# Performance work log

Measured on AMD Instinct MI355X. Metric: run time of the kernel, lower is better.

The kernel has to match this reference:

```python
import jax, jax.numpy as jnp
import numpy as np

B, T, E = 2, 2048, 1024
H = 16
HS = E // H  # 64
EPS = 1e-5


def _ln(x, g, b):
    mu = jnp.mean(x, axis=-1, keepdims=True)
    var = jnp.mean((x - mu) ** 2, axis=-1, keepdims=True)
    return (x - mu) * jax.lax.rsqrt(var + EPS) * g + b


def setup_inputs() -> dict:
    key = jax.random.key(0)
    ks = jax.random.split(key, 12)
    s_e = 1.0 / np.sqrt(E)
    s_h = 1.0 / np.sqrt(H * HS)
    s_f = 1.0 / np.sqrt(4 * E)
    return {
        "x": jax.random.normal(ks[0], (B, T, E), jnp.float32),
        # per-head Q/K/V weights stacked: [H, E, HS] (Linear bias=False)
        "Wq": jax.random.uniform(ks[1], (H, E, HS), jnp.float32, -s_e, s_e),
        "Wk": jax.random.uniform(ks[2], (H, E, HS), jnp.float32, -s_e, s_e),
        "Wv": jax.random.uniform(ks[3], (H, E, HS), jnp.float32, -s_e, s_e),
        # output projection: [H*HS, E]
        "Wp": jax.random.uniform(ks[4], (H * HS, E), jnp.float32, -s_h, s_h),
        "bp": jax.random.uniform(ks[5], (E,), jnp.float32, -s_h, s_h),
        # FFN
        "W1": jax.random.uniform(ks[6], (E, 4 * E), jnp.float32, -s_e, s_e),
        "b1": jax.random.uniform(ks[7], (4 * E,), jnp.float32, -s_e, s_e),
        "W2": jax.random.uniform(ks[8], (4 * E, E), jnp.float32, -s_f, s_f),
        "b2": jax.random.uniform(ks[9], (E,), jnp.float32, -s_f, s_f),
        # LayerNorms
        "g1": jnp.ones((E,), jnp.float32),
        "beta1": jnp.zeros((E,), jnp.float32),
        "g2": jnp.ones((E,), jnp.float32),
        "beta2": jnp.zeros((E,), jnp.float32),
    }


def reference(x, Wq, Wk, Wv, Wp, bp, W1, b1, W2, b2, g1, beta1, g2, beta2):
    # --- pre-LN + multi-head causal self-attention ---
    h = _ln(x, g1, beta1)                                   # [B,T,E]
    Q = jnp.einsum('bte,hed->bhtd', h, Wq)                  # [B,H,T,HS]
    K = jnp.einsum('bte,hed->bhtd', h, Wk)
    V = jnp.einsum('bte,hed->bhtd', h, Wv)
    scores = jnp.einsum('bhtd,bhsd->bhts', Q, K) * (HS ** -0.5)  # [B,H,T,T]
    mask = jnp.tril(jnp.ones((T, T), bool))
    scores = jnp.where(mask, scores, -jnp.inf)
    W = jax.nn.softmax(scores, axis=-1)                     # dropout p=0.0
    out = jnp.einsum('bhts,bhsd->bhtd', W, V)               # [B,H,T,HS]
    out = out.transpose(0, 2, 1, 3).reshape(B, T, H * HS)   # concat heads
    x = x + out @ Wp + bp                                   # residual 1
    # --- pre-LN + FFN ---
    h2 = _ln(x, g2, beta2)
    ff = jax.nn.relu(h2 @ W1 + b1) @ W2 + b2
    return x + ff
```

## Files before the change

kernel.cpp:

```cpp
#include <hip/hip_runtime.h>
#include <math.h>
#include <stdint.h>

typedef unsigned short u16;
typedef __attribute__((ext_vector_type(8))) short bf16x8;
typedef __attribute__((ext_vector_type(4))) float f32x4;

__device__ __forceinline__ u16 f2bf(float f) {
  unsigned int u = __float_as_uint(f);
  u += 0x7FFFu + ((u >> 16) & 1u);
  return (u16)(u >> 16);
}

__global__ __launch_bounds__(256) void transpose_bf16(
    const float* __restrict__ src, u16* __restrict__ dst,
    int R, int C, long sbs, long dbs, int drs, float scale) {
  __shared__ float tile[32][33];
  int c0 = blockIdx.x * 32, r0 = blockIdx.y * 32;
  long sb = (long)blockIdx.z * sbs, db = (long)blockIdx.z * dbs;
  int tx = threadIdx.x & 31, ty = threadIdx.x >> 5;
  #pragma unroll
  for (int k = 0; k < 4; ++k)
    tile[ty + k * 8][tx] = src[sb + (long)(r0 + ty + k * 8) * C + c0 + tx];
  __syncthreads();
  #pragma unroll
  for (int k = 0; k < 4; ++k)
    dst[db + (long)(c0 + ty + k * 8) * drs + r0 + tx] =
        f2bf(tile[tx][ty + k * 8] * scale);
}

__global__ __launch_bounds__(256) void vtrans(
    const u16* __restrict__ QKV, u16* __restrict__ VT) {
  __shared__ u16 Tl[64][72];
  int bt = blockIdx.x, h = blockIdx.y;
  int t = threadIdx.x;
  int r = t >> 3, c0 = (t & 7) << 3;
  const u16* src = QKV + (size_t)(bt * 64 + r) * 3072 + 2048 + h * 64 + c0;
  #pragma unroll
  for (int half = 0; half < 2; ++half) {
    bf16x8 v = *(const bf16x8*)(src + (size_t)(half * 32) * 3072);
    #pragma unroll
    for (int e = 0; e < 8; ++e) Tl[r + half * 32][c0 + e] = (u16)v[e];
  }
  __syncthreads();
  #pragma unroll
  for (int half = 0; half < 2; ++half) {
    int d = (t >> 3) + half * 32, s0 = (t & 7) << 3;
    bf16x8 o;
    #pragma unroll
    for (int e = 0; e < 8; ++e) o[e] = (short)Tl[s0 + e][d];
    *(bf16x8*)(VT + (size_t)(h * 64 + d) * 4096 + bt * 64 + s0) = o;
  }
}

__global__ __launch_bounds__(256) void ln_bf16(
    const float* __restrict__ x, const float* __restrict__ g,
    const float* __restrict__ b, u16* __restrict__ out) {
  int row = blockIdx.x;
  const float* xr = x + (size_t)row * 1024;
  int t = threadIdx.x;
  float4 v = *(const float4*)(xr + t * 4);
  float s = v.x + v.y + v.z + v.w;
  float q = v.x * v.x + v.y * v.y + v.z * v.z + v.w * v.w;
  #pragma unroll
  for (int off = 32; off >= 1; off >>= 1) {
    s += __shfl_xor(s, off);
    q += __shfl_xor(q, off);
  }
  __shared__ float ss[4], qq[4];
  int wid = t >> 6;
  if ((t & 63) == 0) { ss[wid] = s; qq[wid] = q; }
  __syncthreads();
  float st = ss[0] + ss[1] + ss[2] + ss[3];
  float qt = qq[0] + qq[1] + qq[2] + qq[3];
  float mean = st * (1.0f / 1024.0f);
  float var = qt * (1.0f / 1024.0f) - mean * mean;
  float rstd = rsqrtf(var + 1e-5f);
  float4 gv = *(const float4*)(g + t * 4);
  float4 bv = *(const float4*)(b + t * 4);
  u16 o0 = f2bf((v.x - mean) * rstd * gv.x + bv.x);
  u16 o1 = f2bf((v.y - mean) * rstd * gv.y + bv.y);
  u16 o2 = f2bf((v.z - mean) * rstd * gv.z + bv.z);
  u16 o3 = f2bf((v.w - mean) * rstd * gv.w + bv.w);
  uint2 st2;
  st2.x = (unsigned)o0 | ((unsigned)o1 << 16);
  st2.y = (unsigned)o2 | ((unsigned)o3 << 16);
  *(uint2*)(out + (size_t)row * 1024 + t * 4) = st2;
}

template <int BM, int BN>
__global__ __launch_bounds__(256) void gemm_bf16(
    const u16* __restrict__ A, const u16* __restrict__ Bt,
    const float* __restrict__ bias, const float* __restrict__ res,
    float* __restrict__ Cf, u16* __restrict__ Cb,
    int M, int N, int K, int relu) {
  constexpr int MI = BM / 32, NI = BN / 32;
  constexpr int ACH = BM / 32, BCH = BN / 32;
  __shared__ u16 As[2][BM * 64];
  __shared__ u16 Bs[2][BN * 64];
  int tid = threadIdx.x, wave = tid >> 6, lane = tid & 63;
  int wm = wave >> 1, wn = wave & 1;
  int lr = lane & 15, lq = lane >> 4;
  int lrow = lane >> 3, kblk = (lane & 7) ^ (lrow & 7);
  int bn = blockIdx.x * BN, bm = blockIdx.y * BM;
  f32x4 acc[MI][NI];
  #pragma unroll
  for (int i = 0; i < MI; ++i)
    #pragma unroll
    for (int j = 0; j < NI; ++j) acc[i][j] = f32x4{0.f, 0.f, 0.f, 0.f};

  const u16* ag[ACH];
  #pragma unroll
  for (int j = 0; j < ACH; ++j) {
    int c = wave * ACH + j;
    ag[j] = A + (size_t)(bm + c * 8 + lrow) * K + kblk * 8;
  }
  const u16* bg[BCH];
  #pragma unroll
  for (int j = 0; j < BCH; ++j) {
    int c = wave * BCH + j;
    bg[j] = Bt + (size_t)(bn + c * 8 + lrow) * K + kblk * 8;
  }

  bf16x8 ra[ACH], rb[BCH];
  #pragma unroll
  for (int j = 0; j < ACH; ++j) ra[j] = *(const bf16x8*)(ag[j]);
  #pragma unroll
  for (int j = 0; j < BCH; ++j) rb[j] = *(const bf16x8*)(bg[j]);

  int nIter = K >> 6;
  for (int it = 0; it < nIter; ++it) {
    int buf = it & 1;
    #pragma unroll
    for (int j = 0; j < ACH; ++j)
      *(bf16x8*)(&As[buf][(wave * ACH + j) * 512 + lane * 8]) = ra[j];
    #pragma unroll
    for (int j = 0; j < BCH; ++j)
      *(bf16x8*)(&Bs[buf][(wave * BCH + j) * 512 + lane * 8]) = rb[j];
    __syncthreads();
    if (it + 1 < nIter) {
      int k0 = (it + 1) << 6;
      #pragma unroll
      for (int j = 0; j < ACH; ++j) ra[j] = *(const bf16x8*)(ag[j] + k0);
      #pragma unroll
      for (int j = 0; j < BCH; ++j) rb[j] = *(const bf16x8*)(bg[j] + k0);
    }
    #pragma unroll
    for (int kk = 0; kk < 2; ++kk) {
      bf16x8 af[MI], bfr[NI];
      #pragma unroll
      for (int mi = 0; mi < MI; ++mi) {
        int row = wm * (BM / 2) + mi * 16 + lr;
        af[mi] = *(const bf16x8*)(&As[buf][row * 64 + (((kk << 2) + lq) ^ (lr & 7)) * 8]);
      }
      #pragma unroll
      for (int ni = 0; ni < NI; ++ni) {
        int row = wn * (BN / 2) + ni * 16 + lr;
        bfr[ni] = *(const bf16x8*)(&Bs[buf][row * 64 + (((kk << 2) + lq) ^ (lr & 7)) * 8]);
      }
      #pragma unroll
      for (int mi = 0; mi < MI; ++mi)
        #pragma unroll
        for (int ni = 0; ni < NI; ++ni)
          acc[mi][ni] = __builtin_amdgcn_mfma_f32_16x16x32_bf16(af[mi], bfr[ni], acc[mi][ni], 0, 0, 0);
    }
  }

  #pragma unroll
  for (int mi = 0; mi < MI; ++mi) {
    #pragma unroll
    for (int r = 0; r < 4; ++r) {
      int row = bm + wm * (BM / 2) + mi * 16 + lq * 4 + r;
      #pragma unroll
      for (int ni = 0; ni < NI; ++ni) {
        int col = bn + wn * (BN / 2) + ni * 16 + lr;
        float v = acc[mi][ni][r];
        if (bias) v += bias[col];
        if (res) v += res[(size_t)row * N + col];
        if (relu) v = fmaxf(v, 0.f);
        if (Cb) Cb[(size_t)row * N + col] = f2bf(v);
        else Cf[(size_t)row * N + col] = v;
      }
    }
  }
}

__global__ __launch_bounds__(256) void attn_mfma(
    const u16* __restrict__ QKV, const u16* __restrict__ VT,
    u16* __restrict__ O) {
  __shared__ u16 Klds[2][64 * 64];
  __shared__ u16 Vl[2][64 * 64];
  __shared__ u16 Pl[4][16][72];
  int qt = 31 - blockIdx.x;
  int b = blockIdx.y >> 4, hh = blockIdx.y & 15;
  int tid = threadIdx.x, wave = tid >> 6, lane = tid & 63;
  int lr = lane & 15, lq = lane >> 4;
  int lrow = lane >> 3, kb = (lane & 7) ^ (lrow & 7);

  int qrow = qt * 64 + wave * 16 + lr;
  const u16* qp = QKV + (size_t)(b * 2048 + qrow) * 3072 + hh * 64 + lq * 8;
  bf16x8 qf0 = *(const bf16x8*)qp;
  bf16x8 qf1 = *(const bf16x8*)(qp + 32);

  f32x4 of[4];
  float lsum[4];
  #pragma unroll
  for (int i = 0; i < 4; ++i) { of[i] = f32x4{0.f, 0.f, 0.f, 0.f}; lsum[i] = 0.f; }

  const u16* kg[2];
  const u16* vg[2];
  #pragma unroll
  for (int j = 0; j < 2; ++j) {
    int c = wave * 2 + j;
    kg[j] = QKV + (size_t)(b * 2048 + c * 8 + lrow) * 3072 + 1024 + hh * 64 + kb * 8;
    vg[j] = VT + (size_t)(hh * 64 + c * 8 + lrow) * 4096 + b * 2048 + kb * 8;
  }

  bf16x8 rk[2], rv[2];
  #pragma unroll
  for (int j = 0; j < 2; ++j) {
    rk[j] = *(const bf16x8*)(kg[j]);
    rv[j] = *(const bf16x8*)(vg[j]);
  }

  for (int kt = 0; kt <= qt; ++kt) {
    int buf = kt & 1;
    #pragma unroll
    for (int j = 0; j < 2; ++j) {
      *(bf16x8*)(&Klds[buf][(wave * 2 + j) * 512 + lane * 8]) = rk[j];
      *(bf16x8*)(&Vl[buf][(wave * 2 + j) * 512 + lane * 8]) = rv[j];
    }
    __syncthreads();
    if (kt < qt) {
      #pragma unroll
      for (int j = 0; j < 2; ++j) {
        rk[j] = *(const bf16x8*)(kg[j] + (size_t)(kt + 1) * 64 * 3072);
        rv[j] = *(const bf16x8*)(vg[j] + (kt + 1) * 64);
      }
    }

    f32x4 sf[4];
    #pragma unroll
    for (int i = 0; i < 4; ++i) sf[i] = f32x4{0.f, 0.f, 0.f, 0.f};
    #pragma unroll
    for (int ni = 0; ni < 4; ++ni) {
      int row = ni * 16 + lr;
      bf16x8 k0 = *(const bf16x8*)(&Klds[buf][row * 64 + ((lq) ^ (lr & 7)) * 8]);
      bf16x8 k1 = *(const bf16x8*)(&Klds[buf][row * 64 + ((4 + lq) ^ (lr & 7)) * 8]);
      sf[ni] = __builtin_amdgcn_mfma_f32_16x16x32_bf16(qf0, k0, sf[ni], 0, 0, 0);
      sf[ni] = __builtin_amdgcn_mfma_f32_16x16x32_bf16(qf1, k1, sf[ni], 0, 0, 0);
    }
    if (kt == qt) {
      #pragma unroll
      for (int ni = 0; ni < 4; ++ni) {
        int col = ni * 16 + lr;
        #pragma unroll
        for (int r = 0; r < 4; ++r) {
          int row = wave * 16 + lq * 4 + r;
          if (col > row) sf[ni][r] = -1e30f;
        }
      }
    }
    #pragma unroll
    for (int ni = 0; ni < 4; ++ni)
      #pragma unroll
      for (int r = 0; r < 4; ++r) {
        float p = exp2f(sf[ni][r]);
        sf[ni][r] = p;
        lsum[r] += p;
        Pl[wave][lq * 4 + r][ni * 16 + lr] = f2bf(p);
      }
    bf16x8 pa0 = *(const bf16x8*)(&Pl[wave][lr][lq * 8]);
    bf16x8 pa1 = *(const bf16x8*)(&Pl[wave][lr][32 + lq * 8]);
    #pragma unroll
    for (int ni = 0; ni < 4; ++ni) {
      int row = ni * 16 + lr;
      bf16x8 v0 = *(const bf16x8*)(&Vl[buf][row * 64 + ((lq) ^ (lr & 7)) * 8]);
      bf16x8 v1 = *(const bf16x8*)(&Vl[buf][row * 64 + ((4 + lq) ^ (lr & 7)) * 8]);
      of[ni] = __builtin_amdgcn_mfma_f32_16x16x32_bf16(pa0, v0, of[ni], 0, 0, 0);
      of[ni] = __builtin_amdgcn_mfma_f32_16x16x32_bf16(pa1, v1, of[ni], 0, 0, 0);
    }
  }
  #pragma unroll
  for (int r = 0; r < 4; ++r) {
    float l = lsum[r];
    l += __shfl_xor(l, 1);
    l += __shfl_xor(l, 2);
    l += __shfl_xor(l, 4);
    l += __shfl_xor(l, 8);
    float inv = 1.0f / l;
    int row = qt * 64 + wave * 16 + lq * 4 + r;
    u16* op = O + (size_t)(b * 2048 + row) * 1024 + hh * 64;
    #pragma unroll
    for (int ni = 0; ni < 4; ++ni)
      op[ni * 16 + lr] = f2bf(of[ni][r] * inv);
  }
}

extern "C" void kernel_launch(void* const* d_in, const int* in_sizes, int n_in,
                              void* d_out, int out_size, void* d_ws, size_t ws_size,
                              hipStream_t stream) {
  const float* x   = (const float*)d_in[0];
  const float* Wq  = (const float*)d_in[1];
  const float* Wk  = (const float*)d_in[2];
  const float* Wv  = (const float*)d_in[3];
  const float* Wp  = (const float*)d_in[4];
  const float* bp  = (const float*)d_in[5];
  const float* W1  = (const float*)d_in[6];
  const float* b1  = (const float*)d_in[7];
  const float* W2  = (const float*)d_in[8];
  const float* b2  = (const float*)d_in[9];
  const float* g1  = (const float*)d_in[10];
  const float* be1 = (const float*)d_in[11];
  const float* g2  = (const float*)d_in[12];
  const float* be2 = (const float*)d_in[13];
  float* out = (float*)d_out;

  u16* ws16   = (u16*)d_ws;
  u16* Wqkv_t = ws16;
  u16* Wp_t   = Wqkv_t + 3145728;
  u16* W1_t   = Wp_t + 1048576;
  u16* W2_t   = W1_t + 4194304;
  u16* h      = W2_t + 4194304;
  u16* QKV    = h + 4194304;
  u16* Obuf   = QKV + 12582912;
  u16* f      = QKV;
  float* x1   = (float*)(Obuf + 4194304);
  u16* VT     = (u16*)(x1 + 4194304);

  const float qsc = 0.18033688f;
  transpose_bf16<<<dim3(2, 32, 16), 256, 0, stream>>>(Wq, Wqkv_t, 1024, 64, 65536, 65536, 1024, qsc);
  transpose_bf16<<<dim3(2, 32, 16), 256, 0, stream>>>(Wk, Wqkv_t + 1048576, 1024, 64, 65536, 65536, 1024, 1.f);
  transpose_bf16<<<dim3(2, 32, 16), 256, 0, stream>>>(Wv, Wqkv_t + 2097152, 1024, 64, 65536, 65536, 1024, 1.f);
  transpose_bf16<<<dim3(32, 32, 1), 256, 0, stream>>>(Wp, Wp_t, 1024, 1024, 0, 0, 1024, 1.f);
  transpose_bf16<<<dim3(128, 32, 1), 256, 0, stream>>>(W1, W1_t, 1024, 4096, 0, 0, 1024, 1.f);
  transpose_bf16<<<dim3(32, 128, 1), 256, 0, stream>>>(W2, W2_t, 4096, 1024, 0, 0, 4096, 1.f);

  ln_bf16<<<4096, 256, 0, stream>>>(x, g1, be1, h);
  gemm_bf16<128, 128><<<dim3(24, 32), 256, 0, stream>>>(h, Wqkv_t, nullptr, nullptr,
                                                        nullptr, QKV, 4096, 3072, 1024, 0);
  vtrans<<<dim3(64, 16), 256, 0, stream>>>(QKV, VT);
  attn_mfma<<<dim3(32, 32), 256, 0, stream>>>(QKV, VT, Obuf);
  gemm_bf16<128, 64><<<dim3(16, 32), 256, 0, stream>>>(Obuf, Wp_t, bp, x,
                                                       x1, nullptr, 4096, 1024, 1024, 0);
  ln_bf16<<<4096, 256, 0, stream>>>(x1, g2, be2, h);
  gemm_bf16<128, 128><<<dim3(32, 32), 256, 0, stream>>>(h, W1_t, b1, nullptr,
                                                        nullptr, f, 4096, 4096, 1024, 1);
  gemm_bf16<128, 64><<<dim3(16, 32), 256, 0, stream>>>(f, W2_t, b2, x1,
                                                       out, nullptr, 4096, 1024, 4096, 0);
}
```

Baseline: 415.1 us.

## Pair causal attention query tiles, double-buffer GEMM registers, vectorize epilogues

Attention blocks now handle two query tiles (i and 31-i), so every block does the same amount of causal work and each loaded K/V tile serves both. The grid is halved. The GEMM main loop is unrolled by two with two register prefetch sets, loading two k-steps ahead. MFMA operands are swapped so each lane holds four consecutive columns, which allows vectorized bias/residual loads and packed bf16/float4 stores. Rounding changes from round-to-nearest-even to a cheaper add-and-perm packing, and register pressure rises in both kernels.

```diff
diff --git a/kernel.cpp b/kernel.cpp
--- a/kernel.cpp
+++ b/kernel.cpp
@@ -10,6 +10,12 @@
   unsigned int u = __float_as_uint(f);
   u += 0x7FFFu + ((u >> 16) & 1u);
   return (u16)(u >> 16);
+}
+
+__device__ __forceinline__ unsigned pkbf(float a, float b) {
+  unsigned ua = __float_as_uint(a) + 0x8000u;
+  unsigned ub = __float_as_uint(b) + 0x8000u;
+  return __builtin_amdgcn_perm(ub, ua, 0x07060302u);
 }
 
 __global__ __launch_bounds__(256) void transpose_bf16(
@@ -78,13 +84,9 @@
   float rstd = rsqrtf(var + 1e-5f);
   float4 gv = *(const float4*)(g + t * 4);
   float4 bv = *(const float4*)(b + t * 4);
-  u16 o0 = f2bf((v.x - mean) * rstd * gv.x + bv.x);
-  u16 o1 = f2bf((v.y - mean) * rstd * gv.y + bv.y);
-  u16 o2 = f2bf((v.z - mean) * rstd * gv.z + bv.z);
-  u16 o3 = f2bf((v.w - mean) * rstd * gv.w + bv.w);
   uint2 st2;
-  st2.x = (unsigned)o0 | ((unsigned)o1 << 16);
-  st2.y = (unsigned)o2 | ((unsigned)o3 << 16);
+  st2.x = pkbf((v.x - mean) * rstd * gv.x + bv.x, (v.y - mean) * rstd * gv.y + bv.y);
+  st2.y = pkbf((v.z - mean) * rstd * gv.z + bv.z, (v.w - mean) * rstd * gv.w + bv.w);
   *(uint2*)(out + (size_t)row * 1024 + t * 4) = st2;
 }
 
@@ -122,64 +124,75 @@
     bg[j] = Bt + (size_t)(bn + c * 8 + lrow) * K + kblk * 8;
   }
 
-  bf16x8 ra[ACH], rb[BCH];
-  #pragma unroll
-  for (int j = 0; j < ACH; ++j) ra[j] = *(const bf16x8*)(ag[j]);
-  #pragma unroll
-  for (int j = 0; j < BCH; ++j) rb[j] = *(const bf16x8*)(bg[j]);
+  bf16x8 ra0[ACH], ra1[ACH], rb0[BCH], rb1[BCH];
+  #pragma unroll
+  for (int j = 0; j < ACH; ++j) { ra0[j] = *(const bf16x8*)(ag[j]); ra1[j] = *(const bf16x8*)(ag[j] + 64); }
+  #pragma unroll
+  for (int j = 0; j < BCH; ++j) { rb0[j] = *(const bf16x8*)(bg[j]); rb1[j] = *(const bf16x8*)(bg[j] + 64); }
 
   int nIter = K >> 6;
-  for (int it = 0; it < nIter; ++it) {
-    int buf = it & 1;
-    #pragma unroll
-    for (int j = 0; j < ACH; ++j)
-      *(bf16x8*)(&As[buf][(wave * ACH + j) * 512 + lane * 8]) = ra[j];
-    #pragma unroll
-    for (int j = 0; j < BCH; ++j)
-      *(bf16x8*)(&Bs[buf][(wave * BCH + j) * 512 + lane * 8]) = rb[j];
-    __syncthreads();
-    if (it + 1 < nIter) {
-      int k0 = (it + 1) << 6;
-      #pragma unroll
-      for (int j = 0; j < ACH; ++j) ra[j] = *(const bf16x8*)(ag[j] + k0);
-      #pragma unroll
-      for (int j = 0; j < BCH; ++j) rb[j] = *(const bf16x8*)(bg[j] + k0);
-    }
-    #pragma unroll
-    for (int kk = 0; kk < 2; ++kk) {
-      bf16x8 af[MI], bfr[NI];
-      #pragma unroll
-      for (int mi = 0; mi < MI; ++mi) {
-        int row = wm * (BM / 2) + mi * 16 + lr;
-        af[mi] = *(const bf16x8*)(&As[buf][row * 64 + (((kk << 2) + lq) ^ (lr & 7)) * 8]);
-      }
-      #pragma unroll
-      for (int ni = 0; ni < NI; ++ni) {
-        int row = wn * (BN / 2) + ni * 16 + lr;
-        bfr[ni] = *(const bf16x8*)(&Bs[buf][row * 64 + (((kk << 2) + lq) ^ (lr & 7)) * 8]);
-      }
-      #pragma unroll
-      for (int mi = 0; mi < MI; ++mi)
+
+#define GEMM_STEP(BUF, RA, RB, IT)                                                         \
+  {                                                                                        \
+    _Pragma("unroll") for (int j = 0; j < ACH; ++j)                                        \
+        *(bf16x8*)(&As[BUF][(wave * ACH + j) * 512 + lane * 8]) = RA[j];                   \
+    _Pragma("unroll") for (int j = 0; j < BCH; ++j)                                        \
+        *(bf16x8*)(&Bs[BUF][(wave * BCH + j) * 512 + lane * 8]) = RB[j];                   \
+    __syncthreads();                                                                       \
+    if ((IT) + 2 < nIter) {                                                                \
+      int k0 = ((IT) + 2) << 6;                                                            \
+      _Pragma("unroll") for (int j = 0; j < ACH; ++j) RA[j] = *(const bf16x8*)(ag[j] + k0); \
+      _Pragma("unroll") for (int j = 0; j < BCH; ++j) RB[j] = *(const bf16x8*)(bg[j] + k0); \
+    }                                                                                      \
+    _Pragma("unroll") for (int kk = 0; kk < 2; ++kk) {                                     \
+      bf16x8 af[MI], bfr[NI];                                                              \
+      _Pragma("unroll") for (int mi = 0; mi < MI; ++mi)                                    \
+          af[mi] = *(const bf16x8*)(&As[BUF][(wm * (BM / 2) + mi * 16 + lr) * 64 +         \
+                                             (((kk << 2) + lq) ^ (lr & 7)) * 8]);          \
+      _Pragma("unroll") for (int ni = 0; ni < NI; ++ni)                                    \
+          bfr[ni] = *(const bf16x8*)(&Bs[BUF][(wn * (BN / 2) + ni * 16 + lr) * 64 +        \
+                                              (((kk << 2) + lq) ^ (lr & 7)) * 8]);         \
+      _Pragma("unroll") for (int mi = 0; mi < MI; ++mi)                                    \
+          _Pragma("unroll") for (int ni = 0; ni < NI; ++ni)                                \
+              acc[mi][ni] = __builtin_amdgcn_mfma_f32_16x16x32_bf16(bfr[ni], af[mi],       \
+                                                                    acc[mi][ni], 0, 0, 0); \
+    }                                                                                      \
+  }
+
+  for (int it = 0; it < nIter; it += 2) {
+    GEMM_STEP(0, ra0, rb0, it)
+    GEMM_STEP(1, ra1, rb1, it + 1)
+  }
+#undef GEMM_STEP
+
+  #pragma unroll
+  for (int mi = 0; mi < MI; ++mi) {
+    int row = bm + wm * (BM / 2) + mi * 16 + lr;
+    #pragma unroll
+    for (int ni = 0; ni < NI; ++ni) {
+      int col = bn + wn * (BN / 2) + ni * 16 + lq * 4;
+      f32x4 v = acc[mi][ni];
+      if (bias) {
+        float4 bb = *(const float4*)(bias + col);
+        v[0] += bb.x; v[1] += bb.y; v[2] += bb.z; v[3] += bb.w;
+      }
+      if (res) {
+        float4 rv = *(const float4*)(res + (size_t)row * N + col);
+        v[0] += rv.x; v[1] += rv.y; v[2] += rv.z; v[3] += rv.w;
+      }
+      if (relu) {
         #pragma unroll
-        for (int ni = 0; ni < NI; ++ni)
-          acc[mi][ni] = __builtin_amdgcn_mfma_f32_16x16x32_bf16(af[mi], bfr[ni], acc[mi][ni], 0, 0, 0);
-    }
-  }
-
-  #pragma unroll
-  for (int mi = 0; mi < MI; ++mi) {
-    #pragma unroll
-    for (int r = 0; r < 4; ++r) {
-      int row = bm + wm * (BM / 2) + mi * 16 + lq * 4 + r;
-      #pragma unroll
-      for (int ni = 0; ni < NI; ++ni) {
-        int col = bn + wn * (BN / 2) + ni * 16 + lr;
-        float v = acc[mi][ni][r];
-        if (bias) v += bias[col];
-        if (res) v += res[(size_t)row * N + col];
-        if (relu) v = fmaxf(v, 0.f);
-        if (Cb) Cb[(size_t)row * N + col] = f2bf(v);
-        else Cf[(size_t)row * N + col] = v;
+        for (int e = 0; e < 4; ++e) v[e] = fmaxf(v[e], 0.f);
+      }
+      if (Cb) {
+        uint2 w;
+        w.x = pkbf(v[0], v[1]);
+        w.y = pkbf(v[2], v[3]);
+        *(uint2*)(Cb + (size_t)row * N + col) = w;
+      } else {
+        float4 o;
+        o.x = v[0]; o.y = v[1]; o.z = v[2]; o.w = v[3];
+        *(float4*)(Cf + (size_t)row * N + col) = o;
       }
     }
   }
@@ -190,22 +203,28 @@
     u16* __restrict__ O) {
   __shared__ u16 Klds[2][64 * 64];
   __shared__ u16 Vl[2][64 * 64];
-  __shared__ u16 Pl[4][16][72];
-  int qt = 31 - blockIdx.x;
+  __shared__ u16 Pl[4][16 * 72];
+  int i = blockIdx.x;
+  int qtA = i, qtB = 31 - i;
   int b = blockIdx.y >> 4, hh = blockIdx.y & 15;
   int tid = threadIdx.x, wave = tid >> 6, lane = tid & 63;
   int lr = lane & 15, lq = lane >> 4;
   int lrow = lane >> 3, kb = (lane & 7) ^ (lrow & 7);
 
-  int qrow = qt * 64 + wave * 16 + lr;
-  const u16* qp = QKV + (size_t)(b * 2048 + qrow) * 3072 + hh * 64 + lq * 8;
-  bf16x8 qf0 = *(const bf16x8*)qp;
-  bf16x8 qf1 = *(const bf16x8*)(qp + 32);
-
-  f32x4 of[4];
-  float lsum[4];
-  #pragma unroll
-  for (int i = 0; i < 4; ++i) { of[i] = f32x4{0.f, 0.f, 0.f, 0.f}; lsum[i] = 0.f; }
+  const u16* qbase = QKV + (size_t)(b * 2048) * 3072 + hh * 64 + lq * 8;
+  int qrA = qtA * 64 + wave * 16 + lr, qrB = qtB * 64 + wave * 16 + lr;
+  bf16x8 qA0 = *(const bf16x8*)(qbase + (size_t)qrA * 3072);
+  bf16x8 qA1 = *(const bf16x8*)(qbase + (size_t)qrA * 3072 + 32);
+  bf16x8 qB0 = *(const bf16x8*)(qbase + (size_t)qrB * 3072);
+  bf16x8 qB1 = *(const bf16x8*)(qbase + (size_t)qrB * 3072 + 32);
+
+  f32x4 ofA[4], ofB[4];
+  float lA = 0.f, lB = 0.f;
+  #pragma unroll
+  for (int d = 0; d < 4; ++d) {
+    ofA[d] = f32x4{0.f, 0.f, 0.f, 0.f};
+    ofB[d] = f32x4{0.f, 0.f, 0.f, 0.f};
+  }
 
   const u16* kg[2];
   const u16* vg[2];
@@ -215,7 +234,6 @@
     kg[j] = QKV + (size_t)(b * 2048 + c * 8 + lrow) * 3072 + 1024 + hh * 64 + kb * 8;
     vg[j] = VT + (size_t)(hh * 64 + c * 8 + lrow) * 4096 + b * 2048 + kb * 8;
   }
-
   bf16x8 rk[2], rv[2];
   #pragma unroll
   for (int j = 0; j < 2; ++j) {
@@ -223,7 +241,43 @@
     rv[j] = *(const bf16x8*)(vg[j]);
   }
 
-  for (int kt = 0; kt <= qt; ++kt) {
+#define ATTN_TILE(Q0, Q1, QT, OF, LSUM)                                                    \
+  {                                                                                        \
+    f32x4 sf[4];                                                                           \
+    _Pragma("unroll") for (int ni = 0; ni < 4; ++ni) sf[ni] = f32x4{0.f, 0.f, 0.f, 0.f};   \
+    _Pragma("unroll") for (int ni = 0; ni < 4; ++ni) {                                     \
+      int rowk = ni * 16 + lr;                                                             \
+      bf16x8 k0 = *(const bf16x8*)(&Klds[buf][rowk * 64 + ((lq) ^ (lr & 7)) * 8]);         \
+      bf16x8 k1 = *(const bf16x8*)(&Klds[buf][rowk * 64 + ((4 + lq) ^ (lr & 7)) * 8]);     \
+      sf[ni] = __builtin_amdgcn_mfma_f32_16x16x32_bf16(k0, Q0, sf[ni], 0, 0, 0);           \
+      sf[ni] = __builtin_amdgcn_mfma_f32_16x16x32_bf16(k1, Q1, sf[ni], 0, 0, 0);           \
+    }                                                                                      \
+    if (kt == (QT)) {                                                                      \
+      _Pragma("unroll") for (int ni = 0; ni < 4; ++ni)                                     \
+          _Pragma("unroll") for (int r = 0; r < 4; ++r)                                    \
+              if (ni * 16 + lq * 4 + r > wave * 16 + lr) sf[ni][r] = -1e30f;               \
+    }                                                                                      \
+    _Pragma("unroll") for (int ni = 0; ni < 4; ++ni) {                                     \
+      float p0 = exp2f(sf[ni][0]), p1 = exp2f(sf[ni][1]);                                  \
+      float p2 = exp2f(sf[ni][2]), p3 = exp2f(sf[ni][3]);                                  \
+      LSUM += (p0 + p1) + (p2 + p3);                                                       \
+      uint2 w;                                                                             \
+      w.x = pkbf(p0, p1);                                                                  \
+      w.y = pkbf(p2, p3);                                                                  \
+      *(uint2*)(&Pl[wave][lr * 72 + ni * 16 + lq * 4]) = w;                                \
+    }                                                                                      \
+    bf16x8 pf0 = *(const bf16x8*)(&Pl[wave][lr * 72 + lq * 8]);                            \
+    bf16x8 pf1 = *(const bf16x8*)(&Pl[wave][lr * 72 + 32 + lq * 8]);                       \
+    _Pragma("unroll") for (int di = 0; di < 4; ++di) {                                     \
+      int rowv = di * 16 + lr;                                                             \
+      bf16x8 v0 = *(const bf16x8*)(&Vl[buf][rowv * 64 + ((lq) ^ (lr & 7)) * 8]);           \
+      bf16x8 v1 = *(const bf16x8*)(&Vl[buf][rowv * 64 + ((4 + lq) ^ (lr & 7)) * 8]);       \
+      OF[di] = __builtin_amdgcn_mfma_f32_16x16x32_bf16(v0, pf0, OF[di], 0, 0, 0);          \
+      OF[di] = __builtin_amdgcn_mfma_f32_16x16x32_bf16(v1, pf1, OF[di], 0, 0, 0);          \
+    }                                                                                      \
+  }
+
+  for (int kt = 0; kt <= qtB; ++kt) {
     int buf = kt & 1;
     #pragma unroll
     for (int j = 0; j < 2; ++j) {
@@ -231,69 +285,34 @@
       *(bf16x8*)(&Vl[buf][(wave * 2 + j) * 512 + lane * 8]) = rv[j];
     }
     __syncthreads();
-    if (kt < qt) {
+    if (kt < qtB) {
       #pragma unroll
       for (int j = 0; j < 2; ++j) {
         rk[j] = *(const bf16x8*)(kg[j] + (size_t)(kt + 1) * 64 * 3072);
         rv[j] = *(const bf16x8*)(vg[j] + (kt + 1) * 64);
       }
     }
-
-    f32x4 sf[4];
-    #pragma unroll
-    for (int i = 0; i < 4; ++i) sf[i] = f32x4{0.f, 0.f, 0.f, 0.f};
-    #pragma unroll
-    for (int ni = 0; ni < 4; ++ni) {
-      int row = ni * 16 + lr;
-      bf16x8 k0 = *(const bf16x8*)(&Klds[buf][row * 64 + ((lq) ^ (lr & 7)) * 8]);
-      bf16x8 k1 = *(const bf16x8*)(&Klds[buf][row * 64 + ((4 + lq) ^ (lr & 7)) * 8]);
-      sf[ni] = __builtin_amdgcn_mfma_f32_16x16x32_bf16(qf0, k0, sf[ni], 0, 0, 0);
-      sf[ni] = __builtin_amdgcn_mfma_f32_16x16x32_bf16(qf1, k1, sf[ni], 0, 0, 0);
-    }
-    if (kt == qt) {
-      #pragma unroll
-      for (int ni = 0; ni < 4; ++ni) {
-        int col = ni * 16 + lr;
-        #pragma unroll
-        for (int r = 0; r < 4; ++r) {
-          int row = wave * 16 + lq * 4 + r;
-          if (col > row) sf[ni][r] = -1e30f;
-        }
-      }
-    }
-    #pragma unroll
-    for (int ni = 0; ni < 4; ++ni)
-      #pragma unroll
-      for (int r = 0; r < 4; ++r) {
-        float p = exp2f(sf[ni][r]);
-        sf[ni][r] = p;
-        lsum[r] += p;
-        Pl[wave][lq * 4 + r][ni * 16 + lr] = f2bf(p);
-      }
-    bf16x8 pa0 = *(const bf16x8*)(&Pl[wave][lr][lq * 8]);
-    bf16x8 pa1 = *(const bf16x8*)(&Pl[wave][lr][32 + lq * 8]);
-    #pragma unroll
-    for (int ni = 0; ni < 4; ++ni) {
-      int row = ni * 16 + lr;
-      bf16x8 v0 = *(const bf16x8*)(&Vl[buf][row * 64 + ((lq) ^ (lr & 7)) * 8]);
-      bf16x8 v1 = *(const bf16x8*)(&Vl[buf][row * 64 + ((4 + lq) ^ (lr & 7)) * 8]);
-      of[ni] = __builtin_amdgcn_mfma_f32_16x16x32_bf16(pa0, v0, of[ni], 0, 0, 0);
-      of[ni] = __builtin_amdgcn_mfma_f32_16x16x32_bf16(pa1, v1, of[ni], 0, 0, 0);
-    }
-  }
-  #pragma unroll
-  for (int r = 0; r < 4; ++r) {
-    float l = lsum[r];
-    l += __shfl_xor(l, 1);
-    l += __shfl_xor(l, 2);
-    l += __shfl_xor(l, 4);
-    l += __shfl_xor(l, 8);
-    float inv = 1.0f / l;
-    int row = qt * 64 + wave * 16 + lq * 4 + r;
-    u16* op = O + (size_t)(b * 2048 + row) * 1024 + hh * 64;
-    #pragma unroll
-    for (int ni = 0; ni < 4; ++ni)
-      op[ni * 16 + lr] = f2bf(of[ni][r] * inv);
+    ATTN_TILE(qB0, qB1, qtB, ofB, lB)
+    if (kt <= qtA) ATTN_TILE(qA0, qA1, qtA, ofA, lA)
+  }
+#undef ATTN_TILE
+
+  lB += __shfl_xor(lB, 16);
+  lB += __shfl_xor(lB, 32);
+  lA += __shfl_xor(lA, 16);
+  lA += __shfl_xor(lA, 32);
+  float invB = 1.0f / lB, invA = 1.0f / lA;
+  u16* opB = O + (size_t)(b * 2048 + qtB * 64 + wave * 16 + lr) * 1024 + hh * 64;
+  u16* opA = O + (size_t)(b * 2048 + qtA * 64 + wave * 16 + lr) * 1024 + hh * 64;
+  #pragma unroll
+  for (int di = 0; di < 4; ++di) {
+    uint2 wB, wA;
+    wB.x = pkbf(ofB[di][0] * invB, ofB[di][1] * invB);
+    wB.y = pkbf(ofB[di][2] * invB, ofB[di][3] * invB);
+    wA.x = pkbf(ofA[di][0] * invA, ofA[di][1] * invA);
+    wA.y = pkbf(ofA[di][2] * invA, ofA[di][3] * invA);
+    *(uint2*)(opB + di * 16 + lq * 4) = wB;
+    *(uint2*)(opA + di * 16 + lq * 4) = wA;
   }
 }
 
@@ -340,7 +359,7 @@
   gemm_bf16<128, 128><<<dim3(24, 32), 256, 0, stream>>>(h, Wqkv_t, nullptr, nullptr,
                                                         nullptr, QKV, 4096, 3072, 1024, 0);
   vtrans<<<dim3(64, 16), 256, 0, stream>>>(QKV, VT);
-  attn_mfma<<<dim3(32, 32), 256, 0, stream>>>(QKV, VT, Obuf);
+  attn_mfma<<<dim3(16, 32), 256, 0, stream>>>(QKV, VT, Obuf);
   gemm_bf16<128, 64><<<dim3(16, 32), 256, 0, stream>>>(Obuf, Wp_t, bp, x,
                                                        x1, nullptr, 4096, 1024, 1024, 0);
   ln_bf16<<<4096, 256, 0, stream>>>(x1, g2, be2, h);
```

Measured after the change: 350.2 us. 1.19x faster.
